# Performance work log

Hardware: AMD Instinct MI355X
Metric: run time of the kernel (lower is better)

Reference implementation:

```python
import jax, jax.numpy as jnp
import numpy as np

B, S, C = 2, 2048, 2048
N, D = 16, 128          # heads, head_dim
DH = D // 2             # complex half dim = 64
F, H, W = 8, 16, 16     # f_p*h_p*w_p == S
MAX_ROPE = 1024
EPS = 1e-6


def setup_inputs() -> dict:
    key = jax.random.key(0)
    ks = jax.random.split(key, 8)
    # RoPE frequencies as unit complex numbers stored as (cos, sin) pairs.
    t_dim = DH - 2 * (DH // 3)  # 22
    s_dim = DH // 3             # 21
    pos = jnp.arange(MAX_ROPE, dtype=jnp.float32)
    def block(d):
        inv = 1.0 / (10000.0 ** (jnp.arange(d, dtype=jnp.float32) / d))
        return pos[:, None] * inv[None, :]
    ang = jnp.concatenate([block(t_dim), block(s_dim), block(s_dim)], axis=1)  # [MAX_ROPE, DH]
    freqs_cs = jnp.stack([jnp.cos(ang), jnp.sin(ang)], axis=-1).astype(jnp.float32)
    w_scale = 0.02
    return {
        "x": jax.random.normal(ks[0], (B, S, C), jnp.float32),
        "freqs_cs": freqs_cs,
        "wq": jax.random.normal(ks[1], (C, C), jnp.float32) * w_scale,
        "bq": jnp.zeros((C,), jnp.float32),
        "wk": jax.random.normal(ks[2], (C, C), jnp.float32) * w_scale,
        "bk": jnp.zeros((C,), jnp.float32),
        "wv": jax.random.normal(ks[3], (C, C), jnp.float32) * w_scale,
        "bv": jnp.zeros((C,), jnp.float32),
        "wo": jax.random.normal(ks[4], (C, C), jnp.float32) * w_scale,
        "bo": jnp.zeros((C,), jnp.float32),
        "gq": jnp.ones((C,), jnp.float32),
        "gk": jnp.ones((C,), jnp.float32),
        "frame_mask": jnp.ones((B, S), dtype=bool),
        "f_p": F, "h_p": H, "w_p": W,
    }


def _rmsnorm(t, g, eps=EPS):
    return t * jax.lax.rsqrt(jnp.mean(t * t, axis=-1, keepdims=True) + eps) * g


def _rope_volume(freqs_cs, f_p, h_p, w_p):
    # Build per-token (cos, sin) over the 3D grid, matching split/narrow/expand/cat.
    t_dim = DH - 2 * (DH // 3)
    s_dim = DH // 3
    def vol(a):  # a: [MAX_ROPE, DH] -> [S, DH]
        at = jnp.broadcast_to(a[:f_p, None, None, :t_dim], (f_p, h_p, w_p, t_dim))
        ah = jnp.broadcast_to(a[None, :h_p, None, t_dim:t_dim + s_dim], (f_p, h_p, w_p, s_dim))
        aw = jnp.broadcast_to(a[None, None, :w_p, t_dim + s_dim:], (f_p, h_p, w_p, s_dim))
        return jnp.concatenate([at, ah, aw], axis=-1).reshape(f_p * h_p * w_p, DH)
    return vol(freqs_cs[..., 0]), vol(freqs_cs[..., 1])


def _apply_rope(x, cos, sin):
    # x: [B, S, N, D]; complex multiply on interleaved (real, imag) pairs.
    b, s, n, d = x.shape
    xr, xi = x.reshape(b, s, n, DH, 2)[..., 0], x.reshape(b, s, n, DH, 2)[..., 1]
    c = cos[None, :, None, :]
    sn = sin[None, :, None, :]
    out = jnp.stack([xr * c - xi * sn, xr * sn + xi * c], axis=-1)
    return out.reshape(b, s, n, d)


def reference(x, freqs_cs, wq, bq, wk, bk, wv, bv, wo, bo, gq, gk, frame_mask, f_p, h_p, w_p):
    b, s = x.shape[:2]
    m = frame_mask[..., None]  # [B, S, 1]
    q = jnp.where(m, x @ wq.T + bq, 0.0)
    k = jnp.where(m, x @ wk.T + bk, 0.0)
    v = jnp.where(m, x @ wv.T + bv, 0.0)
    q = _rmsnorm(q, gq).reshape(b, s, N, D)
    k = _rmsnorm(k, gk).reshape(b, s, N, D)
    v = v.reshape(b, s, N, D)
    cos, sin = _rope_volume(freqs_cs, f_p, h_p, w_p)
    q = _apply_rope(q, cos, sin)
    k = _apply_rope(k, cos, sin)
    scale = 1.0 / jnp.sqrt(jnp.float32(D))
    scores = jnp.einsum("bqnd,bknd->bnqk", q, k) * scale
    bias = jnp.where(frame_mask[:, None, None, :], 0.0, -1e9).astype(scores.dtype)
    p = jax.nn.softmax(scores + bias, axis=-1)
    out = jnp.einsum("bnqk,bknd->bqnd", p, v)
    out = jnp.where(frame_mask[:, :, None, None], out, 0.0)
    out = out.reshape(b, s, N * D)
    out = out @ wo.T + bo
    return jnp.where(m, out, 0.0)
```

## Files before the change

kernel.cpp:

```cpp
#include <hip/hip_runtime.h>
#include <hip/hip_bf16.h>
#include <stdint.h>


#define S_LEN 2048
#define C_DIM 2048
#define NH    16
#define HD    128

typedef __attribute__((ext_vector_type(8))) short short8;
typedef __attribute__((ext_vector_type(4))) short short4v;
typedef __attribute__((ext_vector_type(4))) float f32x4;

__device__ __forceinline__ short f2bf(float f) {
  union { float f; unsigned u; } a; a.f = f;
  unsigned u = a.u;
  return (short)((u + 0x7fffu + ((u >> 16) & 1u)) >> 16);
}
__device__ __forceinline__ float bf2f(short s) {
  union { float f; unsigned u; } a; a.u = ((unsigned)(unsigned short)s) << 16;
  return a.f;
}

#if defined(__has_builtin)
#if __has_builtin(__builtin_amdgcn_cvt_pk_bf16_f32)
#define HAVE_PK_BF16 1
#endif
#endif
__device__ __forceinline__ unsigned pk_bf16(float a, float b) {
#ifdef HAVE_PK_BF16
  typedef __attribute__((ext_vector_type(2))) __bf16 bf16x2;
  bf16x2 r = __builtin_amdgcn_cvt_pk_bf16_f32(a, b);
  union { bf16x2 v; unsigned u; } c; c.v = r; return c.u;
#else
  return (unsigned)(unsigned short)f2bf(a) | ((unsigned)(unsigned short)f2bf(b) << 16);
#endif
}

__device__ __forceinline__ void gload16(const short* g, short* l) {
  __builtin_amdgcn_global_load_lds((const __attribute__((address_space(1))) void*)g,
                                   (__attribute__((address_space(3))) void*)l,
                                   16, 0, 0);
}

__global__ __launch_bounds__(256) void cvt_bf16(const float* __restrict__ in,
                                                short* __restrict__ out, int n8) {
  int i = blockIdx.x * 256 + threadIdx.x;
  if (i >= n8) return;
  const float4* p = (const float4*)(in + (size_t)i * 8);
  float4 v0 = p[0], v1 = p[1];
  short8 o;
  o[0]=f2bf(v0.x); o[1]=f2bf(v0.y); o[2]=f2bf(v0.z); o[3]=f2bf(v0.w);
  o[4]=f2bf(v1.x); o[5]=f2bf(v1.y); o[6]=f2bf(v1.z); o[7]=f2bf(v1.w);
  *(short8*)(out + (size_t)i * 8) = o;
}

__global__ __launch_bounds__(256) void cvt_bf16_w4(const float* __restrict__ w0,
                                                   const float* __restrict__ w1,
                                                   const float* __restrict__ w2,
                                                   const float* __restrict__ w3,
                                                   short* o0, short* o1, short* o2, short* o3,
                                                   int n8) {
  int y = blockIdx.y;
  const float* in = y == 0 ? w0 : (y == 1 ? w1 : (y == 2 ? w2 : w3));
  short* out = y == 0 ? o0 : (y == 1 ? o1 : (y == 2 ? o2 : o3));
  int i = blockIdx.x * 256 + threadIdx.x;
  if (i >= n8) return;
  const float4* p = (const float4*)(in + (size_t)i * 8);
  float4 v0 = p[0], v1 = p[1];
  short8 o;
  o[0]=f2bf(v0.x); o[1]=f2bf(v0.y); o[2]=f2bf(v0.z); o[3]=f2bf(v0.w);
  o[4]=f2bf(v1.x); o[5]=f2bf(v1.y); o[6]=f2bf(v1.z); o[7]=f2bf(v1.w);
  *(short8*)(out + (size_t)i * 8) = o;
}

__global__ __launch_bounds__(256) void gemm_qkv(const short* __restrict__ A,
                                                const short* __restrict__ Wq,
                                                const short* __restrict__ Wk,
                                                const short* __restrict__ Wv,
                                                const float* __restrict__ bq,
                                                const float* __restrict__ bk,
                                                const float* __restrict__ bv,
                                                short* __restrict__ Oq,
                                                short* __restrict__ Ok,
                                                short* __restrict__ Ovt) {
  __shared__ __align__(16) short As[128 * 64];
  __shared__ __align__(16) short Bs[128 * 64];
  const int tid = threadIdx.x;
  const int w = tid >> 6, lane = tid & 63, quad = lane >> 4, l15 = lane & 15;
  const int wm = w >> 1, wn = w & 1;
  const int m0 = blockIdx.x * 128;
  const int yy = blockIdx.y;
  const int mat = yy >> 4;
  const int n0 = (yy & 15) * 128;
  const short* Bw = mat == 0 ? Wq : (mat == 1 ? Wk : Wv);
  const float* bias = mat == 0 ? bq : (mat == 1 ? bk : bv);

  f32x4 zero = {0.f, 0.f, 0.f, 0.f};
  f32x4 acc[4][4];
#pragma unroll
  for (int i = 0; i < 4; i++)
#pragma unroll
    for (int j = 0; j < 4; j++) acc[i][j] = zero;

  const int lrow = lane >> 3;
  const int lcol = (((lane & 7) ^ lrow) * 8);
  const int sw = (l15 & 7);
  for (int k0 = 0; k0 < C_DIM; k0 += 64) {
    __syncthreads();
#pragma unroll
    for (int t = 0; t < 4; t++) {
      int c = w * 4 + t;
      int row = c * 8 + lrow;
      gload16(A  + (size_t)(m0 + row) * C_DIM + k0 + lcol, &As[c * 512]);
      gload16(Bw + (size_t)(n0 + row) * C_DIM + k0 + lcol, &Bs[c * 512]);
    }
    __syncthreads();
#pragma unroll
    for (int kk = 0; kk < 64; kk += 32) {
      short8 af[4], bf[4];
#pragma unroll
      for (int i = 0; i < 4; i++)
        af[i] = *(const short8*)&As[(wm * 64 + i * 16 + l15) * 64 + ((((kk >> 3) + quad) ^ sw) << 3)];
#pragma unroll
      for (int j = 0; j < 4; j++)
        bf[j] = *(const short8*)&Bs[(wn * 64 + j * 16 + l15) * 64 + ((((kk >> 3) + quad) ^ sw) << 3)];
#pragma unroll
      for (int i = 0; i < 4; i++)
#pragma unroll
        for (int j = 0; j < 4; j++)
          acc[i][j] = __builtin_amdgcn_mfma_f32_16x16x32_bf16(af[i], bf[j], acc[i][j], 0, 0, 0);
    }
  }
  if (mat == 2) {
    const int b = m0 >> 11, sb = (m0 & (S_LEN - 1)) + wm * 64;
#pragma unroll
    for (int j = 0; j < 4; j++) {
      int col = n0 + wn * 64 + j * 16 + l15;
      float bv2 = bias[col];
      int n = col >> 7, d = col & 127;
#pragma unroll
      for (int i = 0; i < 4; i++) {
        int s = sb + i * 16 + quad * 4;
        short4v o;
#pragma unroll
        for (int r = 0; r < 4; r++) o[r] = f2bf(acc[i][j][r] + bv2);
        *(short4v*)(Ovt + ((size_t)(b * NH + n) * HD + d) * S_LEN + s) = o;
      }
    }
  } else {
    short* Oc = mat == 0 ? Oq : Ok;
#pragma unroll
    for (int j = 0; j < 4; j++) {
      int col = n0 + wn * 64 + j * 16 + l15;
      float bv2 = bias[col];
#pragma unroll
      for (int i = 0; i < 4; i++)
#pragma unroll
        for (int r = 0; r < 4; r++) {
          int rowi = m0 + wm * 64 + i * 16 + quad * 4 + r;
          Oc[(size_t)rowi * C_DIM + col] = f2bf(acc[i][j][r] + bv2);
        }
    }
  }
}

__global__ __launch_bounds__(256) void gemm_nt(const short* __restrict__ A,
                                               const short* __restrict__ Bw,
                                               const float* __restrict__ bias,
                                               float* __restrict__ Cc,
                                               int M, int Nn, int K) {
  __shared__ __align__(16) short As[128 * 64];
  __shared__ __align__(16) short Bs[128 * 64];
  const int tid = threadIdx.x;
  const int w = tid >> 6, lane = tid & 63, quad = lane >> 4, l15 = lane & 15;
  const int wm = w >> 1, wn = w & 1;
  const int m0 = blockIdx.x * 128, n0 = blockIdx.y * 128;

  f32x4 zero = {0.f, 0.f, 0.f, 0.f};
  f32x4 acc[4][4];
#pragma unroll
  for (int i = 0; i < 4; i++)
#pragma unroll
    for (int j = 0; j < 4; j++) acc[i][j] = zero;

  const int lrow = lane >> 3;
  const int lcol = (((lane & 7) ^ lrow) * 8);
  const int sw = (l15 & 7);
  for (int k0 = 0; k0 < K; k0 += 64) {
    __syncthreads();
#pragma unroll
    for (int t = 0; t < 4; t++) {
      int c = w * 4 + t;
      int row = c * 8 + lrow;
      gload16(A  + (size_t)(m0 + row) * K + k0 + lcol, &As[c * 512]);
      gload16(Bw + (size_t)(n0 + row) * K + k0 + lcol, &Bs[c * 512]);
    }
    __syncthreads();
#pragma unroll
    for (int kk = 0; kk < 64; kk += 32) {
      short8 af[4], bf[4];
#pragma unroll
      for (int i = 0; i < 4; i++)
        af[i] = *(const short8*)&As[(wm * 64 + i * 16 + l15) * 64 + ((((kk >> 3) + quad) ^ sw) << 3)];
#pragma unroll
      for (int j = 0; j < 4; j++)
        bf[j] = *(const short8*)&Bs[(wn * 64 + j * 16 + l15) * 64 + ((((kk >> 3) + quad) ^ sw) << 3)];
#pragma unroll
      for (int i = 0; i < 4; i++)
#pragma unroll
        for (int j = 0; j < 4; j++)
          acc[i][j] = __builtin_amdgcn_mfma_f32_16x16x32_bf16(af[i], bf[j], acc[i][j], 0, 0, 0);
    }
  }
#pragma unroll
  for (int j = 0; j < 4; j++) {
    int col = n0 + wn * 64 + j * 16 + l15;
    float bv = bias[col];
#pragma unroll
    for (int i = 0; i < 4; i++)
#pragma unroll
      for (int r = 0; r < 4; r++) {
        int rowi = m0 + wm * 64 + i * 16 + quad * 4 + r;
        Cc[(size_t)rowi * Nn + col] = acc[i][j][r] + bv;
      }
  }
}

__global__ __launch_bounds__(256) void rmsrope(const short* __restrict__ qin,
                                               const short* __restrict__ kin,
                                               const float* __restrict__ gq,
                                               const float* __restrict__ gk,
                                               const float* __restrict__ freqs,
                                               short* __restrict__ qout,
                                               short* __restrict__ kout) {
  const int which = blockIdx.y;
  const short* in = which ? kin : qin;
  const float* g = which ? gk : gq;
  short* out = which ? kout : qout;
  const float outscale = which ? 1.0f : 0.08838834764831843f * 1.4426950408889634f;
  const int row = blockIdx.x;
  const int s = row & (S_LEN - 1);
  const short* rp = in + (size_t)row * C_DIM;
  const int tid = threadIdx.x;
  const int e0 = tid * 8;
  short8 sv = *(const short8*)(rp + e0);
  float a[8];
#pragma unroll
  for (int t = 0; t < 8; t++) a[t] = bf2f(sv[t]);
  float ps = 0.f;
#pragma unroll
  for (int t = 0; t < 8; t++) ps += a[t] * a[t];
#pragma unroll
  for (int m = 32; m >= 1; m >>= 1) ps += __shfl_xor(ps, m);
  __shared__ float red[4];
  if ((tid & 63) == 0) red[tid >> 6] = ps;
  __syncthreads();
  float tot = red[0] + red[1] + red[2] + red[3];
  float sc = rsqrtf(tot * (1.0f / 2048.0f) + 1e-6f) * outscale;
  float4 g0 = *(const float4*)(g + e0);
  float4 g1 = *(const float4*)(g + e0 + 4);
  float gg[8] = {g0.x, g0.y, g0.z, g0.w, g1.x, g1.y, g1.z, g1.w};
  const int f = s >> 8, h = (s >> 4) & 15, wv = s & 15;
  short8 o;
#pragma unroll
  for (int q2 = 0; q2 < 4; q2++) {
    int p = (tid & 15) * 4 + q2;
    int pos = p < 22 ? f : (p < 43 ? h : wv);
    float cc = freqs[(pos * 64 + p) * 2];
    float ss = freqs[(pos * 64 + p) * 2 + 1];
    float xr = a[2 * q2] * gg[2 * q2] * sc, xi = a[2 * q2 + 1] * gg[2 * q2 + 1] * sc;
    o[2 * q2]     = f2bf(xr * cc - xi * ss);
    o[2 * q2 + 1] = f2bf(xr * ss + xi * cc);
  }
  *(short8*)(out + (size_t)row * C_DIM + e0) = o;
}

__global__ __launch_bounds__(256, 2) void flash(const short* __restrict__ qb,
                                                const short* __restrict__ kb,
                                                const short* __restrict__ vt,
                                                short* __restrict__ ob) {
  __shared__ __align__(16) short Ks[32 * 512];
  __shared__ __align__(16) short Vs[32 * 512];
  __shared__ __align__(16) short Ps[128 * 64];
  const int tid = threadIdx.x;
  const int w = tid >> 6, lane = tid & 63, quad = lane >> 4, l15 = lane & 15;
  const int bn = blockIdx.y, b = bn >> 4, n = bn & 15;
  const int q0 = blockIdx.x * 128;

  short8 qf[2][4];
#pragma unroll
  for (int i = 0; i < 2; i++)
#pragma unroll
    for (int kc = 0; kc < 4; kc++) {
      int rowq = q0 + w * 32 + i * 16 + l15;
      qf[i][kc] = *(const short8*)(qb + (size_t)(b * S_LEN + rowq) * C_DIM + n * HD + kc * 32 + quad * 8);
    }

  short8 onesf;
#pragma unroll
  for (int t = 0; t < 8; t++) onesf[t] = (l15 == 0) ? (short)0x3f80 : (short)0;

  f32x4 zero = {0.f, 0.f, 0.f, 0.f};
  f32x4 oa[2][9];
#pragma unroll
  for (int i = 0; i < 2; i++)
#pragma unroll
    for (int j = 0; j < 9; j++) oa[i][j] = zero;

  for (int k0 = 0; k0 < S_LEN; k0 += 128) {
    __syncthreads();
#pragma unroll
    for (int jj = 0; jj < 2; jj++) {
      int j = w * 2 + jj;
#pragma unroll
      for (int kc = 0; kc < 4; kc++)
        gload16(kb + (size_t)(b * S_LEN + k0 + j * 16 + l15) * C_DIM + n * HD + kc * 32 + quad * 8,
                &Ks[(j * 4 + kc) * 512]);
    }
#pragma unroll
    for (int jj = 0; jj < 2; jj++) {
      int jd = w * 2 + jj;
#pragma unroll
      for (int kc2 = 0; kc2 < 4; kc2++)
        gload16(vt + (size_t)(bn * HD + jd * 16 + l15) * S_LEN + k0 + kc2 * 32 + quad * 8,
                &Vs[(jd * 4 + kc2) * 512]);
    }
    __syncthreads();

#pragma unroll
    for (int h = 0; h < 2; h++) {
      f32x4 sa[2][4];
#pragma unroll
      for (int i = 0; i < 2; i++)
#pragma unroll
        for (int jp = 0; jp < 4; jp++) sa[i][jp] = zero;
#pragma unroll
      for (int kc = 0; kc < 4; kc++) {
        short8 kf[4];
#pragma unroll
        for (int jp = 0; jp < 4; jp++)
          kf[jp] = *(const short8*)&Ks[((h * 4 + jp) * 4 + kc) * 512 + lane * 8];
#pragma unroll
        for (int i = 0; i < 2; i++)
#pragma unroll
          for (int jp = 0; jp < 4; jp++)
            sa[i][jp] = __builtin_amdgcn_mfma_f32_16x16x32_bf16(qf[i][kc], kf[jp], sa[i][jp], 0, 0, 0);
      }

#pragma unroll
      for (int i = 0; i < 2; i++)
#pragma unroll
        for (int r = 0; r < 4; r++) {
          int m = w * 32 + i * 16 + quad * 4 + r;
#pragma unroll
          for (int jp = 0; jp < 4; jp += 2) {
            float p0 = exp2f(sa[i][jp][r]);
            float p1 = exp2f(sa[i][jp + 1][r]);
            unsigned pp = pk_bf16(p0, p1);
            int c0 = jp * 2 + (l15 >> 3);
            int c1 = c0 + 2;
            Ps[m * 64 + (c0 ^ (m & 7)) * 8 + (l15 & 7)] = (short)pp;
            Ps[m * 64 + (c1 ^ (m & 7)) * 8 + (l15 & 7)] = (short)(pp >> 16);
          }
        }

#pragma unroll
      for (int kc2p = 0; kc2p < 2; kc2p++) {
        int kc2 = h * 2 + kc2p;
        short8 pf[2], vf2[8];
#pragma unroll
        for (int i = 0; i < 2; i++) {
          int m = w * 32 + i * 16 + l15;
          int c = kc2p * 4 + quad;
          pf[i] = *(const short8*)&Ps[m * 64 + (c ^ (m & 7)) * 8];
        }
#pragma unroll
        for (int jd = 0; jd < 8; jd++)
          vf2[jd] = *(const short8*)&Vs[(jd * 4 + kc2) * 512 + lane * 8];
#pragma unroll
        for (int i = 0; i < 2; i++) {
#pragma unroll
          for (int jd = 0; jd < 8; jd++)
            oa[i][jd] = __builtin_amdgcn_mfma_f32_16x16x32_bf16(pf[i], vf2[jd], oa[i][jd], 0, 0, 0);
          oa[i][8] = __builtin_amdgcn_mfma_f32_16x16x32_bf16(pf[i], onesf, oa[i][8], 0, 0, 0);
        }
      }
    }
  }

#pragma unroll
  for (int i = 0; i < 2; i++) {
    float inv[4];
#pragma unroll
    for (int r = 0; r < 4; r++) {
      float lr = __shfl(oa[i][8][r], lane & 48);
      inv[r] = 1.0f / lr;
    }
#pragma unroll
    for (int j = 0; j < 8; j++)
#pragma unroll
      for (int r = 0; r < 4; r++) {
        int rowq = q0 + w * 32 + i * 16 + quad * 4 + r;
        ob[(size_t)(b * S_LEN + rowq) * C_DIM + n * HD + j * 16 + l15] = f2bf(oa[i][j][r] * inv[r]);
      }
  }
}

extern "C" void kernel_launch(void* const* d_in, const int* in_sizes, int n_in,
                              void* d_out, int out_size, void* d_ws, size_t ws_size,
                              hipStream_t stream) {
  const float* x     = (const float*)d_in[0];
  const float* freqs = (const float*)d_in[1];
  const float* wq = (const float*)d_in[2];  const float* bq = (const float*)d_in[3];
  const float* wk = (const float*)d_in[4];  const float* bk = (const float*)d_in[5];
  const float* wv = (const float*)d_in[6];  const float* bv = (const float*)d_in[7];
  const float* wo = (const float*)d_in[8];  const float* bo = (const float*)d_in[9];
  const float* gq = (const float*)d_in[10]; const float* gk = (const float*)d_in[11];
  float* out = (float*)d_out;

  const size_t MS = 4096 * 2048;
  const size_t WS = 2048 * 2048;
  short* xb  = (short*)d_ws;
  short* wqb = xb + MS;
  short* wkb = wqb + WS;
  short* wvb = wkb + WS;
  short* wob = wvb + WS;
  short* q16 = wob + WS;
  short* k16 = q16 + MS;
  short* qbb = k16 + MS;
  short* kbb = qbb + MS;
  short* vtb = kbb + MS;
  short* obb = vtb + MS;

  cvt_bf16<<<dim3((int)(MS / 8 / 256)), dim3(256), 0, stream>>>(x, xb, (int)(MS / 8));
  cvt_bf16_w4<<<dim3((int)(WS / 8 / 256), 4), dim3(256), 0, stream>>>(
      wq, wk, wv, wo, wqb, wkb, wvb, wob, (int)(WS / 8));

  gemm_qkv<<<dim3(32, 48), dim3(256), 0, stream>>>(xb, wqb, wkb, wvb, bq, bk, bv,
                                                   q16, k16, vtb);

  rmsrope<<<dim3(4096, 2), dim3(256), 0, stream>>>(q16, k16, gq, gk, freqs, qbb, kbb);

  flash<<<dim3(16, 32), dim3(256), 0, stream>>>(qbb, kbb, vtb, obb);

  gemm_nt<<<dim3(32, 16), dim3(256), 0, stream>>>(obb, wob, bo, out, 4096, 2048, 2048);
}
```

Before: 443.3 us.

## Rewrite QKV GEMM with 256x256 tiles, 4-stage LDS pipeline and XCD swizzle

Replaces the 128x128 single-buffered QKV GEMM with a 512-thread 256x256-tile kernel. It uses a 4-slot LDS ring with K-step 32, explicit barriers, vmcnt waits and s_setprio around the MFMA bursts. The grid becomes 1D with a block-index swizzle so neighbouring workgroups on the same XCD share tiles. The aim is to overlap global loads with MFMA work and to raise data reuse per tile. In exchange it uses more registers (128 accumulators per lane) and 128KB of LDS, which limits occupancy, and it depends on hand-tuned wait counts being correct.

Result: no change. 451.0 us (+1.7%).

```diff
diff --git a/kernel.cpp b/kernel.cpp
--- a/kernel.cpp
+++ b/kernel.cpp
@@ -74,92 +74,140 @@
   *(short8*)(out + (size_t)i * 8) = o;
 }
 
-__global__ __launch_bounds__(256) void gemm_qkv(const short* __restrict__ A,
-                                                const short* __restrict__ Wq,
-                                                const short* __restrict__ Wk,
-                                                const short* __restrict__ Wv,
-                                                const float* __restrict__ bq,
-                                                const float* __restrict__ bk,
-                                                const float* __restrict__ bv,
-                                                short* __restrict__ Oq,
-                                                short* __restrict__ Ok,
-                                                short* __restrict__ Ovt) {
-  __shared__ __align__(16) short As[128 * 64];
-  __shared__ __align__(16) short Bs[128 * 64];
+#define QKT 32
+#define QNS 64
+
+__global__ __launch_bounds__(512, 2) void gemm_qkv(const short* __restrict__ A,
+                                                   const short* __restrict__ Wq,
+                                                   const short* __restrict__ Wk,
+                                                   const short* __restrict__ Wv,
+                                                   const float* __restrict__ bq,
+                                                   const float* __restrict__ bk,
+                                                   const float* __restrict__ bv,
+                                                   short* __restrict__ Oq,
+                                                   short* __restrict__ Ok,
+                                                   short* __restrict__ Ovt) {
+  __shared__ __align__(16) short As[4 * 8192];
+  __shared__ __align__(16) short Bs[4 * 8192];
   const int tid = threadIdx.x;
   const int w = tid >> 6, lane = tid & 63, quad = lane >> 4, l15 = lane & 15;
-  const int wm = w >> 1, wn = w & 1;
-  const int m0 = blockIdx.x * 128;
-  const int yy = blockIdx.y;
-  const int mat = yy >> 4;
-  const int n0 = (yy & 15) * 128;
+  const int wm = w >> 2, wn = w & 3;
+
+  const int wg = blockIdx.x;
+  const int swz = (wg & 7) * 48 + (wg >> 3);
+  const int m0 = (swz & 15) << 8;
+  const int yy = swz >> 4;
+  const int mat = yy >> 3;
+  const int n0 = (yy & 7) << 8;
   const short* Bw = mat == 0 ? Wq : (mat == 1 ? Wk : Wv);
   const float* bias = mat == 0 ? bq : (mat == 1 ? bk : bv);
 
   f32x4 zero = {0.f, 0.f, 0.f, 0.f};
-  f32x4 acc[4][4];
-#pragma unroll
-  for (int i = 0; i < 4; i++)
+  f32x4 acc[8][4];
+#pragma unroll
+  for (int i = 0; i < 8; i++)
 #pragma unroll
     for (int j = 0; j < 4; j++) acc[i][j] = zero;
 
-  const int lrow = lane >> 3;
-  const int lcol = (((lane & 7) ^ lrow) * 8);
-  const int sw = (l15 & 7);
-  for (int k0 = 0; k0 < C_DIM; k0 += 64) {
-    __syncthreads();
-#pragma unroll
-    for (int t = 0; t < 4; t++) {
-      int c = w * 4 + t;
-      int row = c * 8 + lrow;
-      gload16(A  + (size_t)(m0 + row) * C_DIM + k0 + lcol, &As[c * 512]);
-      gload16(Bw + (size_t)(n0 + row) * C_DIM + k0 + lcol, &Bs[c * 512]);
-    }
-    __syncthreads();
-#pragma unroll
-    for (int kk = 0; kk < 64; kk += 32) {
-      short8 af[4], bf[4];
-#pragma unroll
-      for (int i = 0; i < 4; i++)
-        af[i] = *(const short8*)&As[(wm * 64 + i * 16 + l15) * 64 + ((((kk >> 3) + quad) ^ sw) << 3)];
-#pragma unroll
-      for (int j = 0; j < 4; j++)
-        bf[j] = *(const short8*)&Bs[(wn * 64 + j * 16 + l15) * 64 + ((((kk >> 3) + quad) ^ sw) << 3)];
-#pragma unroll
-      for (int i = 0; i < 4; i++)
-#pragma unroll
-        for (int j = 0; j < 4; j++)
-          acc[i][j] = __builtin_amdgcn_mfma_f32_16x16x32_bf16(af[i], bf[j], acc[i][j], 0, 0, 0);
-    }
-  }
+  const int sub0 = w * 2, sub1 = w * 2 + 1;
+  const int rowoff = lane >> 2;
+  const int xoff = ((lane & 3) ^ ((lane >> 3) & 3)) * 8;
+  const int offA0 = (m0 + sub0 * 16 + rowoff) * C_DIM + xoff;
+  const int offA1 = (m0 + sub1 * 16 + rowoff) * C_DIM + xoff;
+  const int offB0 = (n0 + sub0 * 16 + rowoff) * C_DIM + xoff;
+  const int offB1 = (n0 + sub1 * 16 + rowoff) * C_DIM + xoff;
+  const int cp = (quad ^ ((l15 >> 1) & 3)) * 8;
+  const int laneA = (wm * 128 + l15) * 32 + cp;
+  const int laneB = (wn * 64 + l15) * 32 + cp;
+
+  short8 afrag[4], bfrag[4];
+
+#define BARX do { asm volatile("" ::: "memory"); __builtin_amdgcn_s_barrier(); \
+                  asm volatile("" ::: "memory"); } while (0)
+#define STAGE_A(slot, s) do { \
+    gload16(A + offA0 + (s) * 32, &As[(slot) * 8192 + sub0 * 512]); \
+    gload16(A + offA1 + (s) * 32, &As[(slot) * 8192 + sub1 * 512]); } while (0)
+#define STAGE_B(slot, s) do { \
+    gload16(Bw + offB0 + (s) * 32, &Bs[(slot) * 8192 + sub0 * 512]); \
+    gload16(Bw + offB1 + (s) * 32, &Bs[(slot) * 8192 + sub1 * 512]); } while (0)
+#define LOAD_A(slot, MH) do { _Pragma("unroll") \
+    for (int mf = 0; mf < 4; mf++) \
+      afrag[mf] = *(const short8*)&As[(slot) * 8192 + laneA + ((MH) * 4 + mf) * 512]; } while (0)
+#define LOAD_B(slot) do { _Pragma("unroll") \
+    for (int nf = 0; nf < 4; nf++) \
+      bfrag[nf] = *(const short8*)&Bs[(slot) * 8192 + laneB + nf * 512]; } while (0)
+#define MFMA_H(MH) do { _Pragma("unroll") \
+    for (int mf = 0; mf < 4; mf++) \
+      _Pragma("unroll") \
+      for (int nf = 0; nf < 4; nf++) \
+        acc[(MH) * 4 + mf][nf] = __builtin_amdgcn_mfma_f32_16x16x32_bf16( \
+            afrag[mf], bfrag[nf], acc[(MH) * 4 + mf][nf], 0, 0, 0); } while (0)
+
+#define KTILE(p0, p1, sl3, t, DO3, DO4, DO5, VMC) do { \
+    LOAD_A(p0, 0); LOAD_B(p0); \
+    if (DO3) STAGE_A(sl3, 2 * (t) + 3); \
+    BARX; __builtin_amdgcn_s_setprio(1); MFMA_H(0); __builtin_amdgcn_s_setprio(0); BARX; \
+    LOAD_A(p0, 1); \
+    if (DO4) STAGE_B(p0, 2 * (t) + 4); \
+    BARX; __builtin_amdgcn_s_setprio(1); MFMA_H(1); __builtin_amdgcn_s_setprio(0); BARX; \
+    LOAD_A(p1, 0); LOAD_B(p1); \
+    if (DO4) STAGE_A(p0, 2 * (t) + 4); \
+    BARX; __builtin_amdgcn_s_setprio(1); MFMA_H(0); __builtin_amdgcn_s_setprio(0); BARX; \
+    LOAD_A(p1, 1); \
+    if (DO5) STAGE_B(p1, 2 * (t) + 5); \
+    BARX; __builtin_amdgcn_s_setprio(1); MFMA_H(1); __builtin_amdgcn_s_setprio(0); \
+    asm volatile("s_waitcnt vmcnt(" #VMC ")" ::: "memory"); BARX; \
+  } while (0)
+
+  STAGE_A(0, 0); STAGE_B(0, 0);
+  STAGE_A(1, 1); STAGE_B(1, 1);
+  STAGE_B(2, 2); STAGE_A(2, 2); STAGE_B(3, 3);
+  asm volatile("s_waitcnt vmcnt(6)" ::: "memory");
+  BARX;
+
+  for (int t = 0; t < 30; t += 2) {
+    KTILE(0, 1, 3, t,     1, 1, 1, 6);
+    KTILE(2, 3, 1, t + 1, 1, 1, 1, 6);
+  }
+  KTILE(0, 1, 3, 30, 1, 0, 0, 0);
+  KTILE(2, 3, 1, 31, 0, 0, 0, 0);
+
+#undef KTILE
+#undef MFMA_H
+#undef LOAD_B
+#undef LOAD_A
+#undef STAGE_B
+#undef STAGE_A
+#undef BARX
+
   if (mat == 2) {
-    const int b = m0 >> 11, sb = (m0 & (S_LEN - 1)) + wm * 64;
-#pragma unroll
-    for (int j = 0; j < 4; j++) {
-      int col = n0 + wn * 64 + j * 16 + l15;
+    const int b = m0 >> 11, sb = (m0 & (S_LEN - 1)) + wm * 128;
+#pragma unroll
+    for (int nf = 0; nf < 4; nf++) {
+      int col = n0 + wn * 64 + nf * 16 + l15;
       float bv2 = bias[col];
       int n = col >> 7, d = col & 127;
 #pragma unroll
-      for (int i = 0; i < 4; i++) {
-        int s = sb + i * 16 + quad * 4;
+      for (int mf = 0; mf < 8; mf++) {
+        int s = sb + mf * 16 + quad * 4;
         short4v o;
 #pragma unroll
-        for (int r = 0; r < 4; r++) o[r] = f2bf(acc[i][j][r] + bv2);
+        for (int r = 0; r < 4; r++) o[r] = f2bf(acc[mf][nf][r] + bv2);
         *(short4v*)(Ovt + ((size_t)(b * NH + n) * HD + d) * S_LEN + s) = o;
       }
     }
   } else {
     short* Oc = mat == 0 ? Oq : Ok;
 #pragma unroll
-    for (int j = 0; j < 4; j++) {
-      int col = n0 + wn * 64 + j * 16 + l15;
+    for (int nf = 0; nf < 4; nf++) {
+      int col = n0 + wn * 64 + nf * 16 + l15;
       float bv2 = bias[col];
 #pragma unroll
-      for (int i = 0; i < 4; i++)
+      for (int mf = 0; mf < 8; mf++)
 #pragma unroll
         for (int r = 0; r < 4; r++) {
-          int rowi = m0 + wm * 64 + i * 16 + quad * 4 + r;
-          Oc[(size_t)rowi * C_DIM + col] = f2bf(acc[i][j][r] + bv2);
+          int rowi = m0 + wm * 128 + mf * 16 + quad * 4 + r;
+          Oc[(size_t)rowi * C_DIM + col] = f2bf(acc[mf][nf][r] + bv2);
         }
     }
   }
@@ -437,8 +485,8 @@
   cvt_bf16_w4<<<dim3((int)(WS / 8 / 256), 4), dim3(256), 0, stream>>>(
       wq, wk, wv, wo, wqb, wkb, wvb, wob, (int)(WS / 8));
 
-  gemm_qkv<<<dim3(32, 48), dim3(256), 0, stream>>>(xb, wqb, wkb, wvb, bq, bk, bv,
-                                                   q16, k16, vtb);
+  gemm_qkv<<<dim3(384), dim3(512), 0, stream>>>(xb, wqb, wkb, wvb, bq, bk, bv,
+                                                q16, k16, vtb);
 
   rmsrope<<<dim3(4096, 2), dim3(256), 0, stream>>>(q16, k16, gq, gk, freqs, qbb, kbb);
 
```
